# Optimization experiments

Hardware: AMD Instinct MI355X
Metric: run time of the kernel (lower is better)

The kernel has to match this reference:

```python
import jax, jax.numpy as jnp
import numpy as np

N, E = 50000, 800000
IN_CH, N_HID, OUT_CH = 128, 256, 128
DROPOUT_P = 0.5


def gcn_conv(x, src, dst, ew, W, b, num_nodes):
    # PyG GCNConv with edge_weight: symmetric normalization with self-loops.
    loop = jnp.arange(num_nodes)
    s = jnp.concatenate([src, loop])
    d = jnp.concatenate([dst, loop])
    w = jnp.concatenate([ew, jnp.ones((num_nodes,), ew.dtype)])
    deg = jax.ops.segment_sum(w, d, num_segments=num_nodes)  # [N]
    dinv = jnp.where(deg > 0, jax.lax.rsqrt(deg), 0.0)
    norm = dinv[s] * w * dinv[d]                             # [E+N]
    h = x @ W                                                # [N, out]
    msg = h[s] * norm[:, None]                               # [E+N, out]
    out = jax.ops.segment_sum(msg, d, num_segments=num_nodes)
    return out + b


def setup_inputs() -> dict:
    key = jax.random.key(0)
    ks = jax.random.split(key, 8)
    x = jax.random.normal(ks[0], (N, IN_CH), dtype=jnp.float32)
    edge_index = jax.random.randint(ks[1], (2, E), 0, N, dtype=jnp.int64)
    weight = jax.random.uniform(ks[2], (E,), dtype=jnp.float32)
    # GCNConv params (glorot weights, zero bias)
    s1 = (6.0 / (IN_CH + N_HID)) ** 0.5
    s2 = (6.0 / (N_HID + OUT_CH)) ** 0.5
    W1 = jax.random.uniform(ks[3], (IN_CH, N_HID), jnp.float32, -s1, s1)
    b1 = jnp.zeros((N_HID,), jnp.float32)
    W2 = jax.random.uniform(ks[4], (N_HID, OUT_CH), jnp.float32, -s2, s2)
    b2 = jnp.zeros((OUT_CH,), jnp.float32)
    return {"x": x, "edge_index": edge_index, "weight": weight,
            "W1": W1, "b1": b1, "W2": W2, "b2": b2}


def reference(x, edge_index, weight, W1, b1, W2, b2):
    src, dst = edge_index[0], edge_index[1]
    h = jax.nn.relu(gcn_conv(x, src, dst, weight, W1, b1, N))
    # F.dropout(x, p) with training=True (torch default); fixed key for determinism
    keep = jax.random.bernoulli(jax.random.key(42), 1.0 - DROPOUT_P, h.shape)
    h = jnp.where(keep, h / (1.0 - DROPOUT_P), 0.0)
    return gcn_conv(h, src, dst, weight, W2, b2, N)
```

## Files before the change

### kernel.cpp

```cpp
#include <hip/hip_runtime.h>
#include <hip/hip_bf16.h>
#include <cstdint>

#define INCH 128
#define NHID 256
#define OUTCH 128

typedef unsigned short u16;
typedef unsigned long long u64;
typedef __attribute__((ext_vector_type(8))) short s8v;
typedef __attribute__((ext_vector_type(4))) float f4v;

__device__ __forceinline__ void bsplit(float a, u16& hi, u16& lo) {
    unsigned u = __float_as_uint(a);
    unsigned r = (u + 0x7fffu + ((u >> 16) & 1u)) >> 16;
    hi = (u16)r;
    float res = a - __uint_as_float(r << 16);
    unsigned u2 = __float_as_uint(res);
    lo = (u16)((u2 + 0x7fffu + ((u2 >> 16) & 1u)) >> 16);
}

__device__ __forceinline__ unsigned rotl32(unsigned x, int d) {
    return (x << d) | (x >> (32 - d));
}

__device__ __forceinline__ void threefry2x32(unsigned k0, unsigned k1,
                                             unsigned x0, unsigned x1,
                                             unsigned& o0, unsigned& o1) {
    unsigned ks2 = k0 ^ k1 ^ 0x1BD11BDAu;
#define TF_R(r) { x0 += x1; x1 = rotl32(x1, (r)); x1 ^= x0; }
    x0 += k0; x1 += k1;
    TF_R(13) TF_R(15) TF_R(26) TF_R(6)
    x0 += k1; x1 += ks2 + 1u;
    TF_R(17) TF_R(29) TF_R(16) TF_R(24)
    x0 += ks2; x1 += k0 + 2u;
    TF_R(13) TF_R(15) TF_R(26) TF_R(6)
    x0 += k0; x1 += k1 + 3u;
    TF_R(17) TF_R(29) TF_R(16) TF_R(24)
    x0 += k1; x1 += ks2 + 4u;
    TF_R(13) TF_R(15) TF_R(26) TF_R(6)
    x0 += ks2; x1 += k0 + 5u;
#undef TF_R
    o0 = x0; o1 = x1;
}

__device__ __forceinline__ bool dropout_keep(unsigned j) {
    unsigned o0, o1;
    threefry2x32(0u, 42u, 0u, j, o0, o1);
    return ((o0 ^ o1) & 0x80000000u) == 0u;
}

__global__ void k_init(u64* packed, int N) {
    int i = blockIdx.x * blockDim.x + threadIdx.x;
    if (i < N) packed[i] = 0ull;
}

__global__ void k_hist64(const int4* __restrict__ dst4, const float4* __restrict__ w4,
                         u64* packed, int E4) {
    int i = blockIdx.x * blockDim.x + threadIdx.x;
    if (i < E4) {
        int4 d = dst4[i];
        float4 ww = w4[i];
        const u64 one = 1ull << 32;
        atomicAdd(&packed[d.x], one | (u64)__float2uint_rn(ww.x * 16777216.0f));
        atomicAdd(&packed[d.y], one | (u64)__float2uint_rn(ww.y * 16777216.0f));
        atomicAdd(&packed[d.z], one | (u64)__float2uint_rn(ww.z * 16777216.0f));
        atomicAdd(&packed[d.w], one | (u64)__float2uint_rn(ww.w * 16777216.0f));
    }
}

__global__ void k_dinv_cnt(const u64* __restrict__ packed, float* __restrict__ dinv,
                           int* __restrict__ cnt, int N) {
    int i = blockIdx.x * blockDim.x + threadIdx.x;
    if (i < N) {
        u64 p = packed[i];
        float deg = 1.0f + (float)(unsigned)(p & 0xffffffffull) * (1.0f / 16777216.0f);
        dinv[i] = rsqrtf(deg);
        cnt[i] = (int)(p >> 32);
    }
}

__global__ void scan_block(const int* __restrict__ cnt, int* __restrict__ rowptr,
                           int* __restrict__ bsum, int N) {
    __shared__ int s[256];
    int t = threadIdx.x;
    int i = blockIdx.x * 256 + t;
    int v = (i < N) ? cnt[i] : 0;
    s[t] = v;
    __syncthreads();
    for (int off = 1; off < 256; off <<= 1) {
        int tv = (t >= off) ? s[t - off] : 0;
        __syncthreads();
        s[t] += tv;
        __syncthreads();
    }
    if (i < N) rowptr[i] = s[t] - v;
    if (t == 255) bsum[blockIdx.x] = s[255];
}

__global__ void scan_partials(int* bsum, int nb) {
    __shared__ int s[256];
    int t = threadIdx.x;
    int v = (t < nb) ? bsum[t] : 0;
    s[t] = v;
    __syncthreads();
    for (int off = 1; off < 256; off <<= 1) {
        int tv = (t >= off) ? s[t - off] : 0;
        __syncthreads();
        s[t] += tv;
        __syncthreads();
    }
    if (t < nb) bsum[t] = s[t] - v;
}

__global__ void scan_add(int* rowptr, int* cursor, const int* __restrict__ bsum,
                         int N, int E) {
    int i = blockIdx.x * 256 + threadIdx.x;
    if (i < N) {
        int r = rowptr[i] + bsum[blockIdx.x];
        rowptr[i] = r;
        cursor[i] = r;
    }
    if (i == N) rowptr[N] = E;
}

__global__ void k_place(const int* __restrict__ src, const int* __restrict__ dst,
                        const float* __restrict__ w, const float* __restrict__ dinv,
                        int* cursor, int2* __restrict__ cv, int E) {
    int e = blockIdx.x * blockDim.x + threadIdx.x;
    if (e < E) {
        int s = src[e], d = dst[e];
        float nrm = dinv[s] * w[e] * dinv[d];
        int pos = atomicAdd(&cursor[d], 1);
        cv[pos] = make_int2(s, __float_as_int(nrm));
    }
}

__global__ void conv_wt(const float* __restrict__ W, u16* __restrict__ Wh,
                        u16* __restrict__ Wl, int K, int N) {
    int i = blockIdx.x * 256 + threadIdx.x;
    if (i >= K * N) return;
    int k = i / N, n = i % N;
    u16 hi, lo;
    bsplit(W[i], hi, lo);
    Wh[(size_t)n * K + k] = hi;
    Wl[(size_t)n * K + k] = lo;
}

template <int BN, int WN, bool ACT>
__global__ __launch_bounds__(256) void gemm_mfma(
    const u16* __restrict__ Ah, const u16* __restrict__ Al,
    const u16* __restrict__ Bh, const u16* __restrict__ Bl,
    const float* __restrict__ bias,
    u16* __restrict__ Ch, u16* __restrict__ Cl, float* __restrict__ Cf,
    int M, int Ntot, int K) {
    constexpr int BM = 128;
    constexpr int MFRAG = 4;
    constexpr int NFRAG = WN / 16;
    __shared__ u16 Alh[BM][40], All[BM][40];
    __shared__ u16 Blh[BN][40], Bll[BN][40];

    const int tid = threadIdx.x;
    const int lane = tid & 63;
    const int w = tid >> 6;
    const int wm = (w >> 1) * 64;
    const int wn = (w & 1) * WN;
    const int l15 = lane & 15;
    const int kh = lane >> 4;
    const int row0 = blockIdx.y * BM;
    const int col0 = blockIdx.x * BN;

    f4v acc[MFRAG][NFRAG];
#pragma unroll
    for (int f = 0; f < MFRAG; ++f)
#pragma unroll
        for (int g = 0; g < NFRAG; ++g) acc[f][g] = (f4v){0.f, 0.f, 0.f, 0.f};

    for (int k0 = 0; k0 < K; k0 += 32) {
#pragma unroll
        for (int c = tid; c < BM * 4; c += 256) {
            int m = c >> 2, ko = (c & 3) * 8;
            int gm = row0 + m;
            uint4 vh = make_uint4(0, 0, 0, 0), vl = make_uint4(0, 0, 0, 0);
            if (gm < M) {
                size_t gi = (size_t)gm * K + k0 + ko;
                vh = *reinterpret_cast<const uint4*>(&Ah[gi]);
                vl = *reinterpret_cast<const uint4*>(&Al[gi]);
            }
            *reinterpret_cast<uint4*>(&Alh[m][ko]) = vh;
            *reinterpret_cast<uint4*>(&All[m][ko]) = vl;
        }
#pragma unroll
        for (int c = tid; c < BN * 4; c += 256) {
            int n = c >> 2, ko = (c & 3) * 8;
            size_t gi = (size_t)(col0 + n) * K + k0 + ko;
            *reinterpret_cast<uint4*>(&Blh[n][ko]) = *reinterpret_cast<const uint4*>(&Bh[gi]);
            *reinterpret_cast<uint4*>(&Bll[n][ko]) = *reinterpret_cast<const uint4*>(&Bl[gi]);
        }
        __syncthreads();

        s8v afh[MFRAG], afl[MFRAG], bfh[NFRAG], bfl[NFRAG];
#pragma unroll
        for (int f = 0; f < MFRAG; ++f) {
            afh[f] = *reinterpret_cast<const s8v*>(&Alh[wm + f * 16 + l15][kh * 8]);
            afl[f] = *reinterpret_cast<const s8v*>(&All[wm + f * 16 + l15][kh * 8]);
        }
#pragma unroll
        for (int g = 0; g < NFRAG; ++g) {
            bfh[g] = *reinterpret_cast<const s8v*>(&Blh[wn + g * 16 + l15][kh * 8]);
            bfl[g] = *reinterpret_cast<const s8v*>(&Bll[wn + g * 16 + l15][kh * 8]);
        }
#pragma unroll
        for (int f = 0; f < MFRAG; ++f)
#pragma unroll
            for (int g = 0; g < NFRAG; ++g) {
                acc[f][g] = __builtin_amdgcn_mfma_f32_16x16x32_bf16(afl[f], bfh[g], acc[f][g], 0, 0, 0);
                acc[f][g] = __builtin_amdgcn_mfma_f32_16x16x32_bf16(afh[f], bfl[g], acc[f][g], 0, 0, 0);
                acc[f][g] = __builtin_amdgcn_mfma_f32_16x16x32_bf16(afh[f], bfh[g], acc[f][g], 0, 0, 0);
            }
        __syncthreads();
    }

#pragma unroll
    for (int f = 0; f < MFRAG; ++f) {
#pragma unroll
        for (int g = 0; g < NFRAG; ++g) {
#pragma unroll
            for (int r = 0; r < 4; ++r) {
                int gr = row0 + wm + f * 16 + kh * 4 + r;
                if (gr >= M) continue;
                int gc = col0 + wn + g * 16 + l15;
                float v = acc[f][g][r];
                if (ACT) {
                    v = fmaxf(v + bias[gc], 0.f);
                    unsigned j = (unsigned)gr * (unsigned)Ntot + (unsigned)gc;
                    v = dropout_keep(j) ? v * 2.f : 0.f;
                    u16 hi, lo;
                    bsplit(v, hi, lo);
                    Ch[(size_t)gr * Ntot + gc] = hi;
                    Cl[(size_t)gr * Ntot + gc] = lo;
                } else {
                    Cf[(size_t)gr * Ntot + gc] = v;
                }
            }
        }
    }
}

template <bool SPLIT>
__global__ __launch_bounds__(256) void k_aggregate4(const float4* __restrict__ h4,
                                                    const float* __restrict__ dinv,
                                                    const int* __restrict__ rowptr,
                                                    const int2* __restrict__ cv,
                                                    const float* __restrict__ bias,
                                                    float4* __restrict__ out4,
                                                    u16* __restrict__ outh,
                                                    u16* __restrict__ outl, int N) {
    int node = blockIdx.x * 8 + (threadIdx.x >> 5);
    int lane = threadIdx.x & 31;
    if (node >= N) return;
    float di = dinv[node];
    float s = di * di;
    float4 self = h4[(size_t)node * 32 + lane];
    float4 acc;
    acc.x = self.x * s; acc.y = self.y * s; acc.z = self.z * s; acc.w = self.w * s;
    if (!SPLIT && bias) {
        float4 b = reinterpret_cast<const float4*>(bias)[lane];
        acc.x += b.x; acc.y += b.y; acc.z += b.z; acc.w += b.w;
    }
    int p0 = rowptr[node], p1 = rowptr[node + 1];
    int p = p0;
    for (; p + 8 <= p1; p += 8) {
        int2 e0 = cv[p + 0], e1 = cv[p + 1], e2 = cv[p + 2], e3 = cv[p + 3];
        int2 e4 = cv[p + 4], e5 = cv[p + 5], e6 = cv[p + 6], e7 = cv[p + 7];
        float4 g0 = h4[(size_t)e0.x * 32 + lane];
        float4 g1 = h4[(size_t)e1.x * 32 + lane];
        float4 g2 = h4[(size_t)e2.x * 32 + lane];
        float4 g3 = h4[(size_t)e3.x * 32 + lane];
        float4 g4 = h4[(size_t)e4.x * 32 + lane];
        float4 g5 = h4[(size_t)e5.x * 32 + lane];
        float4 g6 = h4[(size_t)e6.x * 32 + lane];
        float4 g7 = h4[(size_t)e7.x * 32 + lane];
#define ACC(gv, ev) { float v = __int_as_float(ev.y); \
        acc.x = fmaf(gv.x, v, acc.x); acc.y = fmaf(gv.y, v, acc.y); \
        acc.z = fmaf(gv.z, v, acc.z); acc.w = fmaf(gv.w, v, acc.w); }
        ACC(g0, e0) ACC(g1, e1) ACC(g2, e2) ACC(g3, e3)
        ACC(g4, e4) ACC(g5, e5) ACC(g6, e6) ACC(g7, e7)
    }
    for (; p < p1; ++p) {
        int2 e = cv[p];
        float4 g = h4[(size_t)e.x * 32 + lane];
        ACC(g, e)
    }
#undef ACC
    if (SPLIT) {
        ushort4 hv, lv;
        bsplit(acc.x, hv.x, lv.x);
        bsplit(acc.y, hv.y, lv.y);
        bsplit(acc.z, hv.z, lv.z);
        bsplit(acc.w, hv.w, lv.w);
        reinterpret_cast<ushort4*>(outh)[(size_t)node * 32 + lane] = hv;
        reinterpret_cast<ushort4*>(outl)[(size_t)node * 32 + lane] = lv;
    } else {
        out4[(size_t)node * 32 + lane] = acc;
    }
}

extern "C" void kernel_launch(void* const* d_in, const int* in_sizes, int n_in,
                              void* d_out, int out_size, void* d_ws, size_t ws_size,
                              hipStream_t stream) {
    (void)n_in; (void)out_size; (void)ws_size;
    const float* x  = (const float*)d_in[0];
    const int*   ei = (const int*)d_in[1];
    const float* w  = (const float*)d_in[2];
    const float* W1 = (const float*)d_in[3];
    const float* b1 = (const float*)d_in[4];
    const float* W2 = (const float*)d_in[5];
    const float* b2 = (const float*)d_in[6];
    float* out = (float*)d_out;

    int N = in_sizes[0] / INCH;
    int E = in_sizes[1] / 2;
    const int* src = ei;
    const int* dst = ei + E;

    char* ws = (char*)d_ws;
    size_t off = 0;
    auto alloc = [&](size_t bytes) -> char* {
        size_t p = (off + 255) & ~(size_t)255;
        off = p + bytes;
        return ws + p;
    };
    u64*   packed = (u64*)  alloc((size_t)N * 8);
    float* dinv   = (float*)alloc((size_t)N * 4);
    int*   cnt    = (int*)  alloc((size_t)N * 4);
    int*   rowptr = (int*)  alloc((size_t)(N + 1) * 4);
    int*   bsum   = (int*)  alloc(1024);
    int2*  cv     = (int2*) alloc((size_t)E * 8);
    u16*   axh    = (u16*)  alloc((size_t)N * INCH * 2);
    u16*   axl    = (u16*)  alloc((size_t)N * INCH * 2);
    u16*   hdh    = (u16*)  alloc((size_t)N * NHID * 2);
    u16*   hdl    = (u16*)  alloc((size_t)N * NHID * 2);
    u16*   w1h    = (u16*)  alloc((size_t)INCH * NHID * 2);
    u16*   w1l    = (u16*)  alloc((size_t)INCH * NHID * 2);
    u16*   w2h    = (u16*)  alloc((size_t)NHID * OUTCH * 2);
    u16*   w2l    = (u16*)  alloc((size_t)NHID * OUTCH * 2);
    float* g2     = (float*)axh;

    int nb = (N + 255) / 256;
    int eb = (E + 255) / 256;
    int eb4 = (E / 4 + 255) / 256;

    k_init<<<nb, 256, 0, stream>>>(packed, N);
    k_hist64<<<eb4, 256, 0, stream>>>((const int4*)dst, (const float4*)w, packed, E / 4);
    k_dinv_cnt<<<nb, 256, 0, stream>>>(packed, dinv, cnt, N);
    scan_block<<<nb, 256, 0, stream>>>(cnt, rowptr, bsum, N);
    scan_partials<<<1, 256, 0, stream>>>(bsum, nb);
    scan_add<<<nb, 256, 0, stream>>>(rowptr, cnt, bsum, N, E);
    k_place<<<eb, 256, 0, stream>>>(src, dst, w, dinv, cnt, cv, E);
    conv_wt<<<(INCH * NHID + 255) / 256, 256, 0, stream>>>(W1, w1h, w1l, INCH, NHID);
    conv_wt<<<(NHID * OUTCH + 255) / 256, 256, 0, stream>>>(W2, w2h, w2l, NHID, OUTCH);

    int ab = (N + 7) / 8;

    k_aggregate4<true><<<ab, 256, 0, stream>>>((const float4*)x, dinv, rowptr, cv,
                                               nullptr, nullptr, axh, axl, N);
    dim3 gg1(NHID / 128, (N + 127) / 128);
    gemm_mfma<128, 64, true><<<gg1, 256, 0, stream>>>(axh, axl, w1h, w1l, b1,
                                                      hdh, hdl, nullptr, N, NHID, INCH);

    dim3 gg2(OUTCH / 64, (N + 127) / 128);
    gemm_mfma<64, 32, false><<<gg2, 256, 0, stream>>>(hdh, hdl, w2h, w2l, nullptr,
                                                      nullptr, nullptr, g2, N, OUTCH, NHID);
    k_aggregate4<false><<<ab, 256, 0, stream>>>((const float4*)g2, dinv, rowptr, cv,
                                                b2, (float4*)out, nullptr, nullptr, N);
}
```

Before: 377.0 us.

## Precompute dropout mask as bitmask kernel and shrink GEMM row tiles

Moves the threefry dropout RNG out of the GEMM1 epilogue into a separate kernel that writes a packed 1-bit keep mask, which the epilogue then reads per element. The intent is to take the heavy per-element integer hashing off the MFMA kernel's critical path, at the cost of an extra launch and a small mask buffer. Both GEMMs also switch from 128-row to 64-row tiles with recomputed warp layout, giving more blocks for occupancy and load balance. Per-element mask loads in the epilogue are uncoalesced bit reads.

```diff
diff --git a/kernel.cpp b/kernel.cpp
--- a/kernel.cpp
+++ b/kernel.cpp
@@ -44,10 +44,18 @@
     o0 = x0; o1 = x1;
 }
 
-__device__ __forceinline__ bool dropout_keep(unsigned j) {
-    unsigned o0, o1;
-    threefry2x32(0u, 42u, 0u, j, o0, o1);
-    return ((o0 ^ o1) & 0x80000000u) == 0u;
+__global__ __launch_bounds__(256) void k_mask(unsigned* __restrict__ mask, int nwords) {
+    int i = blockIdx.x * 256 + threadIdx.x;
+    if (i >= nwords) return;
+    unsigned base = (unsigned)i * 32u;
+    unsigned m = 0;
+#pragma unroll
+    for (int b = 0; b < 32; ++b) {
+        unsigned o0, o1;
+        threefry2x32(0u, 42u, 0u, base + (unsigned)b, o0, o1);
+        m |= ((((o0 ^ o1) >> 31) ^ 1u) & 1u) << b;
+    }
+    mask[i] = m;
 }
 
 __global__ void k_init(u64* packed, int N) {
@@ -147,15 +155,15 @@
     Wl[(size_t)n * K + k] = lo;
 }
 
-template <int BN, int WN, bool ACT>
+template <int BM, int BN, bool ACT>
 __global__ __launch_bounds__(256) void gemm_mfma(
     const u16* __restrict__ Ah, const u16* __restrict__ Al,
     const u16* __restrict__ Bh, const u16* __restrict__ Bl,
-    const float* __restrict__ bias,
+    const float* __restrict__ bias, const unsigned* __restrict__ mask,
     u16* __restrict__ Ch, u16* __restrict__ Cl, float* __restrict__ Cf,
     int M, int Ntot, int K) {
-    constexpr int BM = 128;
-    constexpr int MFRAG = 4;
+    constexpr int WN = BN / 2;
+    constexpr int MFRAG = BM / 32;
     constexpr int NFRAG = WN / 16;
     __shared__ u16 Alh[BM][40], All[BM][40];
     __shared__ u16 Blh[BN][40], Bll[BN][40];
@@ -163,7 +171,7 @@
     const int tid = threadIdx.x;
     const int lane = tid & 63;
     const int w = tid >> 6;
-    const int wm = (w >> 1) * 64;
+    const int wm = (w >> 1) * (BM / 2);
     const int wn = (w & 1) * WN;
     const int l15 = lane & 15;
     const int kh = lane >> 4;
@@ -234,7 +242,8 @@
                 if (ACT) {
                     v = fmaxf(v + bias[gc], 0.f);
                     unsigned j = (unsigned)gr * (unsigned)Ntot + (unsigned)gc;
-                    v = dropout_keep(j) ? v * 2.f : 0.f;
+                    unsigned keep = (mask[j >> 5] >> (j & 31u)) & 1u;
+                    v = keep ? v * 2.f : 0.f;
                     u16 hi, lo;
                     bsplit(v, hi, lo);
                     Ch[(size_t)gr * Ntot + gc] = hi;
@@ -331,25 +340,27 @@
         off = p + bytes;
         return ws + p;
     };
-    u64*   packed = (u64*)  alloc((size_t)N * 8);
-    float* dinv   = (float*)alloc((size_t)N * 4);
-    int*   cnt    = (int*)  alloc((size_t)N * 4);
-    int*   rowptr = (int*)  alloc((size_t)(N + 1) * 4);
-    int*   bsum   = (int*)  alloc(1024);
-    int2*  cv     = (int2*) alloc((size_t)E * 8);
-    u16*   axh    = (u16*)  alloc((size_t)N * INCH * 2);
-    u16*   axl    = (u16*)  alloc((size_t)N * INCH * 2);
-    u16*   hdh    = (u16*)  alloc((size_t)N * NHID * 2);
-    u16*   hdl    = (u16*)  alloc((size_t)N * NHID * 2);
-    u16*   w1h    = (u16*)  alloc((size_t)INCH * NHID * 2);
-    u16*   w1l    = (u16*)  alloc((size_t)INCH * NHID * 2);
-    u16*   w2h    = (u16*)  alloc((size_t)NHID * OUTCH * 2);
-    u16*   w2l    = (u16*)  alloc((size_t)NHID * OUTCH * 2);
-    float* g2     = (float*)axh;
+    u64*      packed = (u64*)     alloc((size_t)N * 8);
+    float*    dinv   = (float*)   alloc((size_t)N * 4);
+    int*      cnt    = (int*)     alloc((size_t)N * 4);
+    int*      rowptr = (int*)     alloc((size_t)(N + 1) * 4);
+    int*      bsum   = (int*)     alloc(1024);
+    int2*     cv     = (int2*)    alloc((size_t)E * 8);
+    unsigned* mask   = (unsigned*)alloc((size_t)N * NHID / 8);
+    u16*      axh    = (u16*)     alloc((size_t)N * INCH * 2);
+    u16*      axl    = (u16*)     alloc((size_t)N * INCH * 2);
+    u16*      hdh    = (u16*)     alloc((size_t)N * NHID * 2);
+    u16*      hdl    = (u16*)     alloc((size_t)N * NHID * 2);
+    u16*      w1h    = (u16*)     alloc((size_t)INCH * NHID * 2);
+    u16*      w1l    = (u16*)     alloc((size_t)INCH * NHID * 2);
+    u16*      w2h    = (u16*)     alloc((size_t)NHID * OUTCH * 2);
+    u16*      w2l    = (u16*)     alloc((size_t)NHID * OUTCH * 2);
+    float*    g2     = (float*)axh;
 
     int nb = (N + 255) / 256;
     int eb = (E + 255) / 256;
     int eb4 = (E / 4 + 255) / 256;
+    int nwords = N * NHID / 32;
 
     k_init<<<nb, 256, 0, stream>>>(packed, N);
     k_hist64<<<eb4, 256, 0, stream>>>((const int4*)dst, (const float4*)w, packed, E / 4);
@@ -360,17 +371,18 @@
     k_place<<<eb, 256, 0, stream>>>(src, dst, w, dinv, cnt, cv, E);
     conv_wt<<<(INCH * NHID + 255) / 256, 256, 0, stream>>>(W1, w1h, w1l, INCH, NHID);
     conv_wt<<<(NHID * OUTCH + 255) / 256, 256, 0, stream>>>(W2, w2h, w2l, NHID, OUTCH);
+    k_mask<<<(nwords + 255) / 256, 256, 0, stream>>>(mask, nwords);
 
     int ab = (N + 7) / 8;
 
     k_aggregate4<true><<<ab, 256, 0, stream>>>((const float4*)x, dinv, rowptr, cv,
                                                nullptr, nullptr, axh, axl, N);
-    dim3 gg1(NHID / 128, (N + 127) / 128);
-    gemm_mfma<128, 64, true><<<gg1, 256, 0, stream>>>(axh, axl, w1h, w1l, b1,
+    dim3 gg1(NHID / 128, (N + 63) / 64);
+    gemm_mfma<64, 128, true><<<gg1, 256, 0, stream>>>(axh, axl, w1h, w1l, b1, mask,
                                                       hdh, hdl, nullptr, N, NHID, INCH);
 
-    dim3 gg2(OUTCH / 64, (N + 127) / 128);
-    gemm_mfma<64, 32, false><<<gg2, 256, 0, stream>>>(hdh, hdl, w2h, w2l, nullptr,
+    dim3 gg2(OUTCH / 64, (N + 63) / 64);
+    gemm_mfma<64, 64, false><<<gg2, 256, 0, stream>>>(hdh, hdl, w2h, w2l, nullptr, nullptr,
                                                       nullptr, nullptr, g2, N, OUTCH, NHID);
     k_aggregate4<false><<<ab, 256, 0, stream>>>((const float4*)g2, dinv, rowptr, cv,
                                                 b2, (float4*)out, nullptr, nullptr, N);
```

New measurement: 380.7 us. Within noise of the previous version (+1.0%).
